# Performance work log

Hardware: AMD Instinct MI355X
Metric: run time of the kernel (lower is better)

The kernel has to match this reference:

```python
import jax, jax.numpy as jnp
import numpy as np

EPS = 1e-5

def group_norm(x, gamma, beta, groups):
    # x: (B, C, D, H, W)
    B, C = x.shape[0], x.shape[1]
    xr = x.reshape(B, groups, C // groups, -1)
    mean = xr.mean(axis=(2, 3), keepdims=True)
    var = xr.var(axis=(2, 3), keepdims=True)
    xn = ((xr - mean) * jax.lax.rsqrt(var + EPS)).reshape(x.shape)
    return xn * gamma[None, :, None, None, None] + beta[None, :, None, None, None]

def setup_inputs() -> dict:
    key = jax.random.key(0)
    ks = jax.random.split(key, 8)
    B, Ccls = 2, 32
    D = H = W = 64
    s = 0.05
    return {
        "x": jax.random.normal(ks[0], (B, 768, 8, 8, 8), jnp.float32),
        "out": jax.random.normal(ks[1], (B, 48, D, H, W), jnp.float32),
        "task_encoding": jax.random.normal(ks[2], (Ccls, 256, 1, 1, 1), jnp.float32),
        "gn1_g": jnp.ones((768,), jnp.float32),
        "gn1_b": jnp.zeros((768,), jnp.float32),
        "gap_w": jax.random.normal(ks[3], (256, 768), jnp.float32) * s,
        "gap_b": jnp.zeros((256,), jnp.float32),
        "ctrl_w": jax.random.normal(ks[4], (153, 512), jnp.float32) * s,
        "ctrl_b": jnp.zeros((153,), jnp.float32),
        "gn2_g": jnp.ones((48,), jnp.float32),
        "gn2_b": jnp.zeros((48,), jnp.float32),
        "pre_w": jax.random.normal(ks[5], (8, 48), jnp.float32) * s,
        "pre_b": jnp.zeros((8,), jnp.float32),
    }

def reference(x, out, task_encoding, gn1_g, gn1_b, gap_w, gap_b, ctrl_w, ctrl_b,
              gn2_g, gn2_b, pre_w, pre_b):
    B = x.shape[0]
    Ccls = task_encoding.shape[0]
    # GAP branch: GroupNorm(16,768) -> ReLU -> global avg pool -> 1x1x1 conv 768->256
    h = jax.nn.relu(group_norm(x, gn1_g, gn1_b, 16))
    pooled = h.mean(axis=(2, 3, 4))                       # (B, 768)
    x_feat = pooled @ gap_w.T + gap_b                     # (B, 256)
    # Controller: per (batch, class) params from concat(x_feat, task_encoding)
    te = task_encoding.reshape(Ccls, -1)                  # (Ccls, 256)
    params = (jnp.einsum('pf,bf->bp', ctrl_w[:, :256], x_feat)[:, None, :]
              + jnp.einsum('pf,cf->cp', ctrl_w[:, 256:], te)[None, :, :]
              + ctrl_b)                                   # (B, Ccls, 153)
    w1 = params[..., 0:64].reshape(B, Ccls, 8, 8)
    w2 = params[..., 64:128].reshape(B, Ccls, 8, 8)
    w3 = params[..., 128:136].reshape(B, Ccls, 1, 8)
    b1 = params[..., 136:144]
    b2 = params[..., 144:152]
    b3 = params[..., 152:153]
    # precls branch: GroupNorm(16,48) -> ReLU -> 1x1x1 conv 48->8
    g = jax.nn.relu(group_norm(out, gn2_g, gn2_b, 16))
    h0 = jnp.einsum('oc,bcdhw->bodhw', pre_w, g) + pre_b[None, :, None, None, None]
    # Dynamic per-class head: 8->8->8->1 pointwise MLP with ReLU between layers
    t = jax.nn.relu(jnp.einsum('bcij,bjdhw->bcidhw', w1, h0) + b1[..., None, None, None])
    t = jax.nn.relu(jnp.einsum('bcij,bcjdhw->bcidhw', w2, t) + b2[..., None, None, None])
    logits = jnp.einsum('bcij,bcjdhw->bcidhw', w3, t) + b3[..., None, None, None]
    # (B, Ccls, 1, D, H, W) -> (B, Ccls, D, H, W)
    return logits[:, :, 0]
```

## Files before the change

### kernel.cpp

```cpp
#include <hip/hip_runtime.h>

constexpr int NCLS = 32;

constexpr int WS_POOL = 64;
constexpr int WS_XF  = 1600;
constexpr int WS_PAR = 2112;
constexpr int WS_P2  = 11904;

typedef float f2 __attribute__((ext_vector_type(2)));

__device__ __forceinline__ float wred(float v) {
#pragma unroll
  for (int off = 32; off > 0; off >>= 1) v += __shfl_down(v, off, 64);
  return v;
}

__device__ __forceinline__ f2 pfma(float w, f2 v, f2 a) {
  return __builtin_elementwise_fma((f2)w, v, a);
}
__device__ __forceinline__ f2 paff(f2 v, float sc, float sh) {
  return __builtin_elementwise_fma(v, (f2)sc, (f2)sh);
}
__device__ __forceinline__ f2 prelu(f2 a) {
  return __builtin_elementwise_max(a, (f2)0.f);
}

__global__ void k1_stats(const float* __restrict__ x, const float* __restrict__ oin,
                         const float* __restrict__ g1, const float* __restrict__ b1,
                         float* __restrict__ ws) {
  int t = threadIdx.x;
  int wid = t >> 6, lane = t & 63;
  __shared__ float red[8];
  if (blockIdx.x < 768) {
    int blk = blockIdx.x;
    const float4* p = reinterpret_cast<const float4*>(oin + (size_t)blk * 32768);
    float s = 0.f, s2 = 0.f;
#pragma unroll
    for (int k = 0; k < 32; ++k) {
      float4 v = p[k * 256 + t];
      s  += v.x + v.y + v.z + v.w;
      s2 += v.x*v.x + v.y*v.y + v.z*v.z + v.w*v.w;
    }
    s = wred(s); s2 = wred(s2);
    if (lane == 0) { red[wid*2] = s; red[wid*2+1] = s2; }
    __syncthreads();
    if (t == 0) {
      ws[WS_P2 + blk*2]   = red[0]+red[2]+red[4]+red[6];
      ws[WS_P2 + blk*2+1] = red[1]+red[3]+red[5]+red[7];
    }
  } else {
    int g = blockIdx.x - 768;
    __shared__ float mstat[2];
    const float4* p = reinterpret_cast<const float4*>(x + g * 24576);
    float s = 0.f, s2 = 0.f;
#pragma unroll
    for (int k = 0; k < 24; ++k) {
      float4 v = p[k * 256 + t];
      s  += v.x + v.y + v.z + v.w;
      s2 += v.x*v.x + v.y*v.y + v.z*v.z + v.w*v.w;
    }
    s = wred(s); s2 = wred(s2);
    if (lane == 0) { red[wid*2] = s; red[wid*2+1] = s2; }
    __syncthreads();
    if (t == 0) {
      float S  = red[0]+red[2]+red[4]+red[6];
      float S2 = red[1]+red[3]+red[5]+red[7];
      float mean = S * (1.f/24576.f);
      float var  = S2 * (1.f/24576.f) - mean*mean;
      mstat[0] = mean; mstat[1] = rsqrtf(var + 1e-5f);
    }
    __syncthreads();
    float mean = mstat[0], rstd = mstat[1];
#pragma unroll
    for (int k = 0; k < 12; ++k) {
      int i = k*4 + wid;
      int c = (g & 15) * 48 + i;
      float sc = rstd * g1[c];
      float sh = b1[c] - mean * sc;
      const float* q = x + g * 24576 + i * 512;
      float acc = 0.f;
#pragma unroll
      for (int j = 0; j < 8; ++j)
        acc += fmaxf(fmaf(q[lane + j*64], sc, sh), 0.f);
      acc = wred(acc);
      if (lane == 0) ws[WS_POOL + (g >> 4) * 768 + c] = acc * (1.f/512.f);
    }
  }
}

__global__ void k2_xfeat(const float* __restrict__ gapw, const float* __restrict__ gapb,
                         float* __restrict__ ws) {
  int wid = threadIdx.x >> 6, lane = threadIdx.x & 63;
  int idx = blockIdx.x * 4 + wid;
  int b = idx >> 8, o = idx & 255;
  const float* pw = gapw + o * 768;
  const float* pp = ws + WS_POOL + b * 768;
  float s = 0.f;
#pragma unroll
  for (int i = 0; i < 12; ++i) {
    int cc = lane + i*64;
    s += pw[cc] * pp[cc];
  }
  s = wred(s);
  if (lane == 0) ws[WS_XF + idx] = s + gapb[o];
}

__global__ void k3_params(const float* __restrict__ cw, const float* __restrict__ cb,
                          const float* __restrict__ te, float* __restrict__ ws) {
  int wid = threadIdx.x >> 6, lane = threadIdx.x & 63;
  int e = blockIdx.x * 4 + wid;
  int b = e / (NCLS * 153);
  int r = e % (NCLS * 153);
  int c = r / 153, p = r % 153;
  const float* w  = cw + p * 512;
  const float* xf = ws + WS_XF + b * 256;
  const float* tv = te + c * 256;
  float s = 0.f;
#pragma unroll
  for (int i = 0; i < 4; ++i) {
    int f = lane + i*64;
    s += w[f] * xf[f] + w[256 + f] * tv[f];
  }
  s = wred(s);
  if (lane == 0) ws[WS_PAR + e] = s + cb[p];
}

__global__ __launch_bounds__(256) void k4_main(const float* __restrict__ oin,
                                               const float* __restrict__ prew,
                                               const float* __restrict__ preb,
                                               const float* __restrict__ g2,
                                               const float* __restrict__ b2,
                                               const float* __restrict__ ws,
                                               float* __restrict__ out) {
  __shared__ __align__(16) float Wl[NCLS * 160];
  __shared__ __align__(16) float prewT[384];
  __shared__ float2 ssl[48];
  __shared__ float ms[64];
  int t = threadIdx.x;
  int b    = blockIdx.x >> 8;
  int tile = blockIdx.x & 255;

  if (t < 32) {
    float S = 0.f, S2 = 0.f;
#pragma unroll
    for (int k = 0; k < 24; ++k) {
      S  += ws[WS_P2 + (t*24 + k)*2];
      S2 += ws[WS_P2 + (t*24 + k)*2 + 1];
    }
    float mean = S * (1.f/786432.f);
    float var  = S2 * (1.f/786432.f) - mean*mean;
    ms[t*2] = mean; ms[t*2+1] = rsqrtf(var + 1e-5f);
  }
  if (t < 128) {
#pragma unroll
    for (int k = 0; k < 3; ++k) {
      int i = t + k*128;
      prewT[(i % 48) * 8 + (i / 48)] = prew[i];
    }
  }
  {
    const float* wsrc = ws + WS_PAR + (size_t)b * NCLS * 153;
#pragma unroll 4
    for (int cc = 0; cc < NCLS; ++cc)
      if (t < 153) Wl[cc*160 + t] = wsrc[cc*153 + t];
  }
  __syncthreads();
  if (t < 48) {
    int grp = (b << 4) + t / 3;
    float mean = ms[grp*2], rstd = ms[grp*2+1];
    float sc = rstd * g2[t];
    ssl[t] = make_float2(sc, b2[t] - mean * sc);
  }
  __syncthreads();

  const float4* ip4 = reinterpret_cast<const float4*>(oin)
                      + (size_t)b * 48 * 65536 + tile*256 + t;
  const float4* pT4 = reinterpret_cast<const float4*>(prewT);
  f2 h0[8][2];
#pragma unroll
  for (int o = 0; o < 8; ++o) {
    float pb = preb[o];
    h0[o][0] = (f2)pb; h0[o][1] = (f2)pb;
  }
#pragma unroll 8
  for (int c = 0; c < 48; ++c) {
    float4 v = ip4[(size_t)c * 65536];
    float2 ss = ssl[c];
    f2 g0 = prelu(paff((f2){v.x, v.y}, ss.x, ss.y));
    f2 g1 = prelu(paff((f2){v.z, v.w}, ss.x, ss.y));
    float4 w0 = pT4[c*2], w1 = pT4[c*2+1];
    float wv[8] = {w0.x, w0.y, w0.z, w0.w, w1.x, w1.y, w1.z, w1.w};
#pragma unroll
    for (int o = 0; o < 8; ++o) {
      h0[o][0] = pfma(wv[o], g0, h0[o][0]);
      h0[o][1] = pfma(wv[o], g1, h0[o][1]);
    }
  }

  float4* op4 = reinterpret_cast<float4*>(out)
                + (size_t)b * NCLS * 65536 + tile*256 + t;
#pragma unroll 1
  for (int cls = 0; cls < NCLS; ++cls) {
    const float* Wc = Wl + cls * 160;
    f2 t1[8][2];
#pragma unroll
    for (int i = 0; i < 8; ++i) {
      float bi = Wc[136 + i];
      f2 a0 = (f2)bi, a1 = (f2)bi;
#pragma unroll
      for (int j = 0; j < 8; ++j) {
        float w = Wc[i*8 + j];
        a0 = pfma(w, h0[j][0], a0);
        a1 = pfma(w, h0[j][1], a1);
      }
      t1[i][0] = prelu(a0); t1[i][1] = prelu(a1);
    }
    float b3v = Wc[152];
    f2 lg0 = (f2)b3v, lg1 = (f2)b3v;
#pragma unroll
    for (int i = 0; i < 8; ++i) {
      float bi = Wc[144 + i];
      f2 a0 = (f2)bi, a1 = (f2)bi;
#pragma unroll
      for (int j = 0; j < 8; ++j) {
        float w = Wc[64 + i*8 + j];
        a0 = pfma(w, t1[j][0], a0);
        a1 = pfma(w, t1[j][1], a1);
      }
      a0 = prelu(a0); a1 = prelu(a1);
      float w3 = Wc[128 + i];
      lg0 = pfma(w3, a0, lg0);
      lg1 = pfma(w3, a1, lg1);
    }
    op4[(size_t)cls * 65536] = make_float4(lg0.x, lg0.y, lg1.x, lg1.y);
  }
}

extern "C" void kernel_launch(void* const* d_in, const int* in_sizes, int n_in,
                              void* d_out, int out_size, void* d_ws, size_t ws_size,
                              hipStream_t stream) {
  const float* x    = (const float*)d_in[0];
  const float* oin  = (const float*)d_in[1];
  const float* te   = (const float*)d_in[2];
  const float* g1   = (const float*)d_in[3];
  const float* b1   = (const float*)d_in[4];
  const float* gapw = (const float*)d_in[5];
  const float* gapb = (const float*)d_in[6];
  const float* cw   = (const float*)d_in[7];
  const float* cb   = (const float*)d_in[8];
  const float* g2   = (const float*)d_in[9];
  const float* b2   = (const float*)d_in[10];
  const float* prew = (const float*)d_in[11];
  const float* preb = (const float*)d_in[12];
  float* ws  = (float*)d_ws;
  float* out = (float*)d_out;

  hipLaunchKernelGGL(k1_stats,  dim3(800),  dim3(256), 0, stream, x, oin, g1, b1, ws);
  hipLaunchKernelGGL(k2_xfeat,  dim3(128),  dim3(256), 0, stream, gapw, gapb, ws);
  hipLaunchKernelGGL(k3_params, dim3(2448), dim3(256), 0, stream, cw, cb, te, ws);
  hipLaunchKernelGGL(k4_main,   dim3(512),  dim3(256), 0, stream, oin, prew, preb, g2, b2, ws, out);
}
```

Baseline: 271.8 us.

## Software-pipeline per-class weight LDS loads into registers in the dynamic head loop

Per-class MLP weights are now loaded from LDS as float4 vectors into register arrays. The next class's first-layer weights are prefetched while the current class's second layer computes, with sched_barriers and empty asm pins forcing the order. Launch bounds add a minimum of 2 blocks per CU to cap register use. The aim is to hide LDS latency and cut scalar LDS reads, at the cost of heavy register pressure (about 160 extra VGPRs) and possible spills.

After: 267.7 us. No clear change (-1.5%).

```diff
diff --git a/kernel.cpp b/kernel.cpp
--- a/kernel.cpp
+++ b/kernel.cpp
@@ -23,6 +23,11 @@
 }
 __device__ __forceinline__ f2 prelu(f2 a) {
   return __builtin_elementwise_max(a, (f2)0.f);
+}
+
+#define PINF(x) asm volatile("" : "+v"(x))
+__device__ __forceinline__ void pin4(float4& v) {
+  PINF(v.x); PINF(v.y); PINF(v.z); PINF(v.w);
 }
 
 __global__ void k1_stats(const float* __restrict__ x, const float* __restrict__ oin,
@@ -125,13 +130,13 @@
   if (lane == 0) ws[WS_PAR + e] = s + cb[p];
 }
 
-__global__ __launch_bounds__(256) void k4_main(const float* __restrict__ oin,
-                                               const float* __restrict__ prew,
-                                               const float* __restrict__ preb,
-                                               const float* __restrict__ g2,
-                                               const float* __restrict__ b2,
-                                               const float* __restrict__ ws,
-                                               float* __restrict__ out) {
+__global__ __launch_bounds__(256, 2) void k4_main(const float* __restrict__ oin,
+                                                  const float* __restrict__ prew,
+                                                  const float* __restrict__ preb,
+                                                  const float* __restrict__ g2,
+                                                  const float* __restrict__ b2,
+                                                  const float* __restrict__ ws,
+                                                  float* __restrict__ out) {
   __shared__ __align__(16) float Wl[NCLS * 160];
   __shared__ __align__(16) float prewT[384];
   __shared__ float2 ssl[48];
@@ -199,38 +204,77 @@
 
   float4* op4 = reinterpret_cast<float4*>(out)
                 + (size_t)b * NCLS * 65536 + tile*256 + t;
+
+  float4 w1A[18];
+  {
+    const float4* W0 = reinterpret_cast<const float4*>(Wl);
+#pragma unroll
+    for (int k = 0; k < 16; ++k) w1A[k] = W0[k];
+    w1A[16] = W0[34]; w1A[17] = W0[35];
+  }
+
 #pragma unroll 1
   for (int cls = 0; cls < NCLS; ++cls) {
-    const float* Wc = Wl + cls * 160;
+#pragma unroll
+    for (int k = 0; k < 18; ++k) pin4(w1A[k]);
+    __builtin_amdgcn_sched_barrier(0);
+
+    const float4* W4 = reinterpret_cast<const float4*>(Wl + cls * 160);
+    float4 Bv[21];
+#pragma unroll
+    for (int k = 0; k < 16; ++k) Bv[k] = W4[16 + k];
+    Bv[16] = W4[32]; Bv[17] = W4[33];
+    Bv[18] = W4[36]; Bv[19] = W4[37];
+    Bv[20] = W4[38];
+    __builtin_amdgcn_sched_barrier(0);
+
+    float b1arr[8] = {w1A[16].x, w1A[16].y, w1A[16].z, w1A[16].w,
+                      w1A[17].x, w1A[17].y, w1A[17].z, w1A[17].w};
     f2 t1[8][2];
 #pragma unroll
     for (int i = 0; i < 8; ++i) {
-      float bi = Wc[136 + i];
-      f2 a0 = (f2)bi, a1 = (f2)bi;
+      float4 wa = w1A[i*2], wb = w1A[i*2+1];
+      float wv[8] = {wa.x, wa.y, wa.z, wa.w, wb.x, wb.y, wb.z, wb.w};
+      f2 a0 = (f2)b1arr[i], a1 = (f2)b1arr[i];
 #pragma unroll
       for (int j = 0; j < 8; ++j) {
-        float w = Wc[i*8 + j];
-        a0 = pfma(w, h0[j][0], a0);
-        a1 = pfma(w, h0[j][1], a1);
+        a0 = pfma(wv[j], h0[j][0], a0);
+        a1 = pfma(wv[j], h0[j][1], a1);
       }
       t1[i][0] = prelu(a0); t1[i][1] = prelu(a1);
     }
-    float b3v = Wc[152];
+
+#pragma unroll
+    for (int k = 0; k < 21; ++k) pin4(Bv[k]);
+    __builtin_amdgcn_sched_barrier(0);
+
+    {
+      const float4* Wn = reinterpret_cast<const float4*>(Wl + ((cls + 1) & (NCLS - 1)) * 160);
+#pragma unroll
+      for (int k = 0; k < 16; ++k) w1A[k] = Wn[k];
+      w1A[16] = Wn[34]; w1A[17] = Wn[35];
+    }
+    __builtin_amdgcn_sched_barrier(0);
+
+    float b2arr[8] = {Bv[18].x, Bv[18].y, Bv[18].z, Bv[18].w,
+                      Bv[19].x, Bv[19].y, Bv[19].z, Bv[19].w};
+    float w3arr[8] = {Bv[16].x, Bv[16].y, Bv[16].z, Bv[16].w,
+                      Bv[17].x, Bv[17].y, Bv[17].z, Bv[17].w};
+    float b3v = Bv[20].x;
     f2 lg0 = (f2)b3v, lg1 = (f2)b3v;
 #pragma unroll
     for (int i = 0; i < 8; ++i) {
-      float bi = Wc[144 + i];
-      f2 a0 = (f2)bi, a1 = (f2)bi;
+      float4 wa = Bv[i*2], wb = Bv[i*2+1];
+      float wv[8] = {wa.x, wa.y, wa.z, wa.w, wb.x, wb.y, wb.z, wb.w};
+      f2 a0 = (f2)b2arr[i], a1 = (f2)b2arr[i];
 #pragma unroll
       for (int j = 0; j < 8; ++j) {
-        float w = Wc[64 + i*8 + j];
-        a0 = pfma(w, t1[j][0], a0);
-        a1 = pfma(w, t1[j][1], a1);
+        a0 = pfma(wv[j], t1[j][0], a0);
+        a1 = pfma(wv[j], t1[j][1], a1);
       }
       a0 = prelu(a0); a1 = prelu(a1);
-      float w3 = Wc[128 + i];
-      lg0 = pfma(w3, a0, lg0);
-      lg1 = pfma(w3, a1, lg1);
+      lg0 = pfma(w3arr[i], a0, lg0);
+      lg1 = pfma(w3arr[i], a1, lg1);
     }
     op4[(size_t)cls * 65536] = make_float4(lg0.x, lg0.y, lg1.x, lg1.y);
   }
```
